# Kernel tuning notes

Hardware: AMD Instinct MI355X
Metric: run time of the kernel (lower is better)

## Reference

```python
import jax, jax.numpy as jnp
import numpy as np

DEPTH = 10


def setup_inputs() -> dict:
    key = jax.random.key(0)
    k1, k2, k3, k4 = jax.random.split(key, 4)
    B, C_in, O, D, L = 4096, 512, 1024, DEPTH, 2 ** DEPTH
    x = jax.random.normal(k1, (B, C_in), dtype=jnp.float32)
    thresholds = 6.0 * jax.random.uniform(k2, (O, D), dtype=jnp.float32) - 3.0
    ordinals = jax.random.randint(k3, (O, D), 0, C_in, dtype=jnp.int64)
    weights = jax.random.normal(k4, (O, L), dtype=jnp.float32)
    return {"x": x, "thresholds": thresholds, "ordinals": ordinals, "weights": weights}


def reference(x, thresholds, ordinals, weights):
    # x: [B, C_in]; thresholds/ordinals: [O, D]; weights: [O, 2**D]
    O, D = thresholds.shape
    # Gather the D decision features for each fern: [B, O, D]
    feats = x[:, ordinals]
    margins = feats - thresholds[None, :, :]
    # Leaf index from sign bits (bit d is MSB-first): [B, O]
    powers = (2 ** (D - 1 - jnp.arange(D))).astype(jnp.int32)
    bits = (margins > 0).astype(jnp.int32)
    leaf = jnp.sum(bits * powers, axis=-1)
    # Hinge value: minimum absolute margin along the path: [B, O]
    min_margin = jnp.min(jnp.abs(margins), axis=-1)
    # Select leaf weight per (batch, fern): w[o, leaf[b, o]]
    w_sel = jnp.take_along_axis(weights[None, :, :], leaf[:, :, None], axis=2)[..., 0]
    return w_sel * min_margin  # [B, O]
```

## Files before the change

kernel.cpp:

```cpp
#include <hip/hip_runtime.h>


#define B_TOT  4096
#define CIN    512
#define O_TOT  1024
#define DEPTH  10
#define LEAVES 1024
#define OSH_LD 522

typedef float vf4 __attribute__((ext_vector_type(4)));
typedef float vf2 __attribute__((ext_vector_type(2)));

__global__ __launch_bounds__(256, 4) void transpose_kernel(
    const float* __restrict__ x,
    float* __restrict__ xT)
{
    __shared__ float tile[64 * 64];
    const int t  = threadIdx.x;
    const int c0 = blockIdx.x * 64;
    const int r0 = blockIdx.y * 64;

#pragma unroll
    for (int k = 0; k < 4; ++k) {
        const int id = k * 256 + t;
        const int r  = id >> 4;
        const int c4 = id & 15;
        const vf4 v = *reinterpret_cast<const vf4*>(
            x + (size_t)(r0 + r) * CIN + c0 + (c4 << 2));
        const int c = c4 << 2;
        tile[r * 64 + ((c + 0) ^ r)] = v.x;
        tile[r * 64 + ((c + 1) ^ r)] = v.y;
        tile[r * 64 + ((c + 2) ^ r)] = v.z;
        tile[r * 64 + ((c + 3) ^ r)] = v.w;
    }
    __syncthreads();

#pragma unroll
    for (int k = 0; k < 4; ++k) {
        const int id = k * 256 + t;
        const int c  = id >> 4;
        const int j4 = id & 15;
        vf4 v;
        v.x = tile[(j4 * 4 + 0) * 64 + (c ^ (j4 * 4 + 0))];
        v.y = tile[(j4 * 4 + 1) * 64 + (c ^ (j4 * 4 + 1))];
        v.z = tile[(j4 * 4 + 2) * 64 + (c ^ (j4 * 4 + 2))];
        v.w = tile[(j4 * 4 + 3) * 64 + (c ^ (j4 * 4 + 3))];
        *reinterpret_cast<vf4*>(xT + (size_t)(c0 + c) * B_TOT + r0 + (j4 << 2)) = v;
    }
}

__global__ __launch_bounds__(1024, 4) void fern_kernel(
    const float* __restrict__ xT,
    const float* __restrict__ thresholds,
    const int*   __restrict__ ordinals,
    const float* __restrict__ weights,
    float*       __restrict__ out)
{
    __shared__ float wlds[8 * LEAVES];
    __shared__ float osh[16 * OSH_LD];

    const int t    = threadIdx.x;
    const int lane = t & 63;
    const int wv   = __builtin_amdgcn_readfirstlane(t >> 6);

    const int id = blockIdx.x;
    const int b0 = (id & 7) * 512;
    const int o0 = (id >> 3) * 16;

#pragma unroll
    for (int p = 0; p < 2; ++p) {
        const vf4* wsrc = reinterpret_cast<const vf4*>(
            weights + (size_t)(o0 + p * 8) * LEAVES);
        vf4* wdst = reinterpret_cast<vf4*>(wlds);
#pragma unroll
        for (int k = 0; k < 2; ++k)
            wdst[k * 1024 + t] = wsrc[k * 1024 + t];
        __syncthreads();

#pragma unroll
        for (int q = 0; q < 2; ++q) {
            const int task = wv * 2 + q;
            const int oi   = task >> 2;
            const int ch   = task & 3;
            const int o    = o0 + p * 8 + oi;
            const int*   op = ordinals   + o * DEPTH;
            const float* tp = thresholds + o * DEPTH;
            const int bb = b0 + ch * 128 + 2 * lane;

            vf2 xv[DEPTH];
#pragma unroll
            for (int d = 0; d < DEPTH; ++d)
                xv[d] = *reinterpret_cast<const vf2*>(
                    xT + (size_t)op[d] * B_TOT + bb);

            int   leaf0 = 0, leaf1 = 0;
            float mm0 = 1e30f, mm1 = 1e30f;
#pragma unroll
            for (int d = 0; d < DEPTH; ++d) {
                const float thr = tp[d];
                const float g0  = xv[d].x - thr;
                const float g1  = xv[d].y - thr;
                leaf0 = (leaf0 << 1) | (g0 > 0.0f ? 1 : 0);
                leaf1 = (leaf1 << 1) | (g1 > 0.0f ? 1 : 0);
                mm0   = fminf(mm0, fabsf(g0));
                mm1   = fminf(mm1, fabsf(g1));
            }
            vf2 r;
            r.x = wlds[oi * LEAVES + leaf0] * mm0;
            r.y = wlds[oi * LEAVES + leaf1] * mm1;
            *reinterpret_cast<vf2*>(
                &osh[(p * 8 + oi) * OSH_LD + ch * 128 + 2 * lane]) = r;
        }
        __syncthreads();
    }

#pragma unroll
    for (int k = 0; k < 2; ++k) {
        const int i  = k * 1024 + t;
        const int b  = i >> 2;
        const int oq = (i & 3) << 2;
        vf4 v;
        v.x = osh[(oq + 0) * OSH_LD + b];
        v.y = osh[(oq + 1) * OSH_LD + b];
        v.z = osh[(oq + 2) * OSH_LD + b];
        v.w = osh[(oq + 3) * OSH_LD + b];
        __builtin_nontemporal_store(v, reinterpret_cast<vf4*>(
            out + (size_t)(b0 + b) * O_TOT + o0 + oq));
    }
}

extern "C" void kernel_launch(void* const* d_in, const int* in_sizes, int n_in,
                              void* d_out, int out_size, void* d_ws, size_t ws_size,
                              hipStream_t stream) {
    const float* x          = (const float*)d_in[0];
    const float* thresholds = (const float*)d_in[1];
    const int*   ordinals   = (const int*)d_in[2];
    const float* weights    = (const float*)d_in[3];
    float*       out        = (float*)d_out;
    float*       xT         = (float*)d_ws;

    dim3 tg(CIN / 64, B_TOT / 64);
    transpose_kernel<<<tg, 256, 0, stream>>>(x, xT);

    fern_kernel<<<512, 1024, 0, stream>>>(xT, thresholds, ordinals, weights, out);
}
```

Measured before the change: 90.64 us.

## Shrink fern blocks, drop LDS weight staging, gather weights directly from global

Blocks change from 1024 threads covering 16 ferns × 512 samples to 256 threads covering 16 ferns × 256 samples. Each thread now handles 4 samples with vf4 loads instead of 2. The shared-memory staging of leaf weights and its barrier are removed; leaf weights are gathered straight from global memory, relying on L2/L1 caching. Block index mapping is remapped to group blocks for locality, and LDS use drops, which should allow more resident blocks. The cost is scattered global gathers for the weights in place of LDS reads.

```diff
diff --git a/kernel.cpp b/kernel.cpp
--- a/kernel.cpp
+++ b/kernel.cpp
@@ -6,10 +6,9 @@
 #define O_TOT  1024
 #define DEPTH  10
 #define LEAVES 1024
-#define OSH_LD 522
+#define OSH_LD 268
 
 typedef float vf4 __attribute__((ext_vector_type(4)));
-typedef float vf2 __attribute__((ext_vector_type(2)));
 
 __global__ __launch_bounds__(256, 4) void transpose_kernel(
     const float* __restrict__ x,
@@ -49,14 +48,13 @@
     }
 }
 
-__global__ __launch_bounds__(1024, 4) void fern_kernel(
+__global__ __launch_bounds__(256, 4) void fern_kernel(
     const float* __restrict__ xT,
     const float* __restrict__ thresholds,
     const int*   __restrict__ ordinals,
     const float* __restrict__ weights,
     float*       __restrict__ out)
 {
-    __shared__ float wlds[8 * LEAVES];
     __shared__ float osh[16 * OSH_LD];
 
     const int t    = threadIdx.x;
@@ -64,59 +62,49 @@
     const int wv   = __builtin_amdgcn_readfirstlane(t >> 6);
 
     const int id = blockIdx.x;
-    const int b0 = (id & 7) * 512;
-    const int o0 = (id >> 3) * 16;
+    const int k  = id & 7;
+    const int j  = id >> 3;
+    const int b0 = ((k & 3) * 4 + (j & 3)) * 256;
+    const int o0 = ((k >> 2) * 32 + (j >> 2)) * 16;
+    const int bb = b0 + 4 * lane;
 
 #pragma unroll
-    for (int p = 0; p < 2; ++p) {
-        const vf4* wsrc = reinterpret_cast<const vf4*>(
-            weights + (size_t)(o0 + p * 8) * LEAVES);
-        vf4* wdst = reinterpret_cast<vf4*>(wlds);
+    for (int i = 0; i < 4; ++i) {
+        const int ol = wv * 4 + i;
+        const int o  = o0 + ol;
+        const int*   op = ordinals   + o * DEPTH;
+        const float* tp = thresholds + o * DEPTH;
+
+        vf4 xv[DEPTH];
 #pragma unroll
-        for (int k = 0; k < 2; ++k)
-            wdst[k * 1024 + t] = wsrc[k * 1024 + t];
-        __syncthreads();
+        for (int d = 0; d < DEPTH; ++d)
+            xv[d] = *reinterpret_cast<const vf4*>(
+                xT + (size_t)op[d] * B_TOT + bb);
+
+        int   leaf[4] = {0, 0, 0, 0};
+        float mm[4]   = {1e30f, 1e30f, 1e30f, 1e30f};
+#pragma unroll
+        for (int d = 0; d < DEPTH; ++d) {
+            const float thr = tp[d];
+#pragma unroll
+            for (int u = 0; u < 4; ++u) {
+                const float g = xv[d][u] - thr;
+                leaf[u] = (leaf[u] << 1) | (g > 0.0f ? 1 : 0);
+                mm[u]   = fminf(mm[u], fabsf(g));
+            }
+        }
+        const float* wrow = weights + (size_t)o * LEAVES;
+        vf4 r;
+#pragma unroll
+        for (int u = 0; u < 4; ++u)
+            r[u] = wrow[leaf[u]] * mm[u];
+        *reinterpret_cast<vf4*>(&osh[ol * OSH_LD + 4 * lane]) = r;
+    }
+    __syncthreads();
 
 #pragma unroll
-        for (int q = 0; q < 2; ++q) {
-            const int task = wv * 2 + q;
-            const int oi   = task >> 2;
-            const int ch   = task & 3;
-            const int o    = o0 + p * 8 + oi;
-            const int*   op = ordinals   + o * DEPTH;
-            const float* tp = thresholds + o * DEPTH;
-            const int bb = b0 + ch * 128 + 2 * lane;
-
-            vf2 xv[DEPTH];
-#pragma unroll
-            for (int d = 0; d < DEPTH; ++d)
-                xv[d] = *reinterpret_cast<const vf2*>(
-                    xT + (size_t)op[d] * B_TOT + bb);
-
-            int   leaf0 = 0, leaf1 = 0;
-            float mm0 = 1e30f, mm1 = 1e30f;
-#pragma unroll
-            for (int d = 0; d < DEPTH; ++d) {
-                const float thr = tp[d];
-                const float g0  = xv[d].x - thr;
-                const float g1  = xv[d].y - thr;
-                leaf0 = (leaf0 << 1) | (g0 > 0.0f ? 1 : 0);
-                leaf1 = (leaf1 << 1) | (g1 > 0.0f ? 1 : 0);
-                mm0   = fminf(mm0, fabsf(g0));
-                mm1   = fminf(mm1, fabsf(g1));
-            }
-            vf2 r;
-            r.x = wlds[oi * LEAVES + leaf0] * mm0;
-            r.y = wlds[oi * LEAVES + leaf1] * mm1;
-            *reinterpret_cast<vf2*>(
-                &osh[(p * 8 + oi) * OSH_LD + ch * 128 + 2 * lane]) = r;
-        }
-        __syncthreads();
-    }
-
-#pragma unroll
-    for (int k = 0; k < 2; ++k) {
-        const int i  = k * 1024 + t;
+    for (int kk = 0; kk < 4; ++kk) {
+        const int i  = kk * 256 + t;
         const int b  = i >> 2;
         const int oq = (i & 3) << 2;
         vf4 v;
@@ -142,5 +130,5 @@
     dim3 tg(CIN / 64, B_TOT / 64);
     transpose_kernel<<<tg, 256, 0, stream>>>(x, xT);
 
-    fern_kernel<<<512, 1024, 0, stream>>>(xT, thresholds, ordinals, weights, out);
+    fern_kernel<<<1024, 256, 0, stream>>>(xT, thresholds, ordinals, weights, out);
 }
```

Result: faster. 86.33 us (-4.7%).
